# Performance work log

Hardware: AMD Instinct MI355X
Metric: run time of the kernel (lower is better)

## Reference

```python
import jax, jax.numpy as jnp
import numpy as np

B, S, H = 8, 2048, 1024

def setup_inputs() -> dict:
    key = jax.random.key(0)
    k1, k2 = jax.random.split(key)
    inputs = jax.random.normal(k1, (B, S, H), dtype=jnp.float32)
    # PyTorch Linear weight [out, in]; init ~ U(-1/sqrt(H), 1/sqrt(H)) approximated with scaled normal
    W = jax.random.normal(k2, (H, H), dtype=jnp.float32) * (1.0 / np.sqrt(H))
    b = jnp.zeros((H,), dtype=jnp.float32)
    return {"inputs": inputs, "W": W, "b": b}

def reference(inputs, W, b):
    # QW = inputs @ W^T + b   (nn.Linear)
    QW = jnp.einsum('bsh,oh->bso', inputs, W) + b  # [B,S,H]
    # score = QW @ inputs^T  (no scaling, no mask)
    score = jnp.einsum('bqh,bkh->bqk', QW, inputs)  # [B,S,S]
    attn = jax.nn.softmax(score, axis=2)
    # output = attn @ inputs
    output = jnp.einsum('bqk,bkh->bqh', attn, inputs)  # [B,S,H]
    return output
```

## Files before the change

kernel.cpp:

```cpp
#include <hip/hip_runtime.h>
#include <hip/hip_bf16.h>
#include <hip/hip_fp16.h>

typedef unsigned short u16;
typedef __attribute__((ext_vector_type(8))) _Float16 f16x8;
typedef __attribute__((ext_vector_type(4))) float f32x4;

#define B_ 8
#define S_ 2048
#define H_ 1024
#define M_ (B_ * S_)

__device__ __forceinline__ u16 f2h(float f) {
  _Float16 h = (_Float16)f;
  return __builtin_bit_cast(u16, h);
}

__global__ void f32_to_f16_kernel(const float* __restrict__ x,
                                  u16* __restrict__ o, int n4) {
  int stride = gridDim.x * blockDim.x;
  for (int i = blockIdx.x * blockDim.x + threadIdx.x; i < n4; i += stride) {
    float4 v = reinterpret_cast<const float4*>(x)[i];
    ushort4 h;
    h.x = f2h(v.x); h.y = f2h(v.y); h.z = f2h(v.z); h.w = f2h(v.w);
    reinterpret_cast<ushort4*>(o)[i] = h;
  }
}

__global__ void transpose_f32_kernel(const float* __restrict__ x,
                                     u16* __restrict__ xt) {
  __shared__ u16 t[64][65];
  int b = blockIdx.z, s0 = blockIdx.x * 64, h0 = blockIdx.y * 64;
  int tx = threadIdx.x, ty = threadIdx.y;
  const float* src = x + ((size_t)b * S_ + s0) * H_ + h0;
#pragma unroll
  for (int i = 0; i < 4; ++i)
    t[ty + 16 * i][tx] = f2h(src[(size_t)(ty + 16 * i) * H_ + tx]);
  __syncthreads();
  u16* dst = xt + ((size_t)b * H_ + h0) * S_ + s0;
#pragma unroll
  for (int i = 0; i < 4; ++i)
    dst[(size_t)(ty + 16 * i) * S_ + tx] = t[tx][ty + 16 * i];
}

__device__ __forceinline__ void async_stage16(const u16* g, u16* l) {
  __builtin_amdgcn_global_load_lds(
      (__attribute__((address_space(1))) void*)g,
      (__attribute__((address_space(3))) void*)l, 16, 0, 0);
}

template <int OM>
__global__ __launch_bounds__(512) void gemm8_kernel(
    const u16* __restrict__ A, const u16* __restrict__ B,
    float* __restrict__ Cf, u16* __restrict__ Ch,
    const float* __restrict__ bias,
    int lda, int ldb, int ldc, int K,
    long sAz, long sBz, long sCz) {
  __shared__ __align__(16) u16 sA[2][256 * 64];
  __shared__ __align__(16) u16 sB[2][256 * 64];

  int gx = gridDim.x, gy = gridDim.y;
  int nwg = gx * gy * gridDim.z;
  int wgid = blockIdx.x + gx * (blockIdx.y + gy * blockIdx.z);
  int q = nwg >> 3, r = nwg & 7;
  int xcd = wgid & 7, idx = wgid >> 3;
  int nid = (xcd < r ? xcd * (q + 1) : r * (q + 1) + (xcd - r) * q) + idx;
  int bxi = nid % gx, t2 = nid / gx;
  int byi = t2 % gy, bzi = t2 / gy;

  int tid = threadIdx.x, wave = tid >> 6, lane = tid & 63;
  int wm = wave >> 2, wn = wave & 3;
  int bm = bxi * 256, bn = byi * 256;
  long zA = (long)bzi * sAz;
  long zB = (long)bzi * sBz;
  long zC = (long)bzi * sCz;
  const u16* gA = A + zA + (size_t)bm * lda;
  const u16* gB = B + zB + (size_t)bn * ldb;

  int srow = tid >> 3;
  int scolb = (tid & 7) << 4;
  int sco = (scolb ^ ((srow & 7) << 4)) >> 1;
  size_t aO0 = (size_t)srow * lda + sco, aO1 = aO0 + (size_t)64 * lda;
  size_t bO0 = (size_t)srow * ldb + sco, bO1 = bO0 + (size_t)64 * ldb;
  int ld0 = srow * 64 + (scolb >> 1), ld1 = ld0 + 64 * 64;

  auto stgA = [&](int slot, int half, int kofs) {
    const u16* g = gA + (size_t)(half * 128) * lda + kofs;
    u16* l = &sA[slot][half * 8192];
    async_stage16(g + aO0, l + ld0);
    async_stage16(g + aO1, l + ld1);
  };
  auto stgB = [&](int slot, int half, int kofs) {
    const u16* g = gB + (size_t)(half * 128) * ldb + kofs;
    u16* l = &sB[slot][half * 8192];
    async_stage16(g + bO0, l + ld0);
    async_stage16(g + bO1, l + ld1);
  };

  int la = lane & 15;
  int kg = (lane >> 4) << 4;
  auto frag = [&](const u16* base, int row, int colb) -> f16x8 {
    int off = (row << 7) + (colb ^ ((row & 7) << 4));
    return *reinterpret_cast<const f16x8*>(
        reinterpret_cast<const char*>(base) + off);
  };

  f16x8 aF[4][2], bF[2][2];
  f32x4 acc[8][4] = {};

  auto RA = [&](int slot, int qm) {
#pragma unroll
    for (int j = 0; j < 4; ++j)
#pragma unroll
      for (int ks = 0; ks < 2; ++ks)
        aF[j][ks] = frag(sA[slot], qm * 128 + (j * 2 + wm) * 16 + la,
                         ks * 64 + kg);
  };
  auto RB = [&](int slot, int qn) {
#pragma unroll
    for (int i = 0; i < 2; ++i)
#pragma unroll
      for (int ks = 0; ks < 2; ++ks)
        bF[i][ks] = frag(sB[slot], qn * 128 + (i * 4 + wn) * 16 + la,
                         ks * 64 + kg);
  };
  auto MM = [&](int qm, int qn) {
#pragma unroll
    for (int ks = 0; ks < 2; ++ks)
#pragma unroll
      for (int j = 0; j < 4; ++j)
#pragma unroll
        for (int i = 0; i < 2; ++i)
          acc[qm * 4 + j][qn * 2 + i] = __builtin_amdgcn_mfma_f32_16x16x32_f16(
              aF[j][ks], bF[i][ks], acc[qm * 4 + j][qn * 2 + i], 0, 0, 0);
  };

#define VM4 asm volatile("s_waitcnt vmcnt(4)" ::: "memory")
#define VM2 asm volatile("s_waitcnt vmcnt(2)" ::: "memory")
#define BAR __builtin_amdgcn_s_barrier()
#define LG0                                              \
  asm volatile("s_waitcnt lgkmcnt(0)" ::: "memory");     \
  __builtin_amdgcn_sched_barrier(0)
#define MFMA_CL(qm, qn)                 \
  __builtin_amdgcn_s_setprio(1);        \
  MM(qm, qn);                           \
  __builtin_amdgcn_s_setprio(0)

  stgA(0, 0, 0); stgB(0, 0, 0); stgA(0, 1, 0); stgB(0, 1, 0);
  VM4;
  BAR;

  int NI = K >> 7;
  for (int it = 0; it < NI; ++it) {
    int k1 = (2 * it + 1) << 6, k2 = (2 * it + 2) << 6;
    bool more = (it + 1 < NI);
    RA(0, 0); RB(0, 0); stgA(1, 0, k1);
    BAR; LG0; MFMA_CL(0, 0); VM2; BAR;
    RA(0, 1); stgB(1, 0, k1);
    BAR; LG0; MFMA_CL(1, 0); BAR;
    RB(0, 1); stgA(1, 1, k1);
    BAR; LG0; MFMA_CL(1, 1); BAR;
    RA(0, 0); stgB(1, 1, k1);
    BAR; LG0; MFMA_CL(0, 1); VM4; BAR;
    RA(1, 0); RB(1, 0); if (more) stgA(0, 0, k2);
    BAR; LG0; MFMA_CL(0, 0); VM2; BAR;
    RA(1, 1); if (more) stgB(0, 0, k2);
    BAR; LG0; MFMA_CL(1, 0); BAR;
    RB(1, 1); if (more) stgA(0, 1, k2);
    BAR; LG0; MFMA_CL(1, 1); BAR;
    RA(1, 0); if (more) stgB(0, 1, k2);
    BAR; LG0; MFMA_CL(0, 1); VM4; BAR;
  }
#undef VM4
#undef VM2
#undef BAR
#undef LG0
#undef MFMA_CL

#pragma unroll
  for (int mf = 0; mf < 8; ++mf) {
    int qm = mf >> 2, j = mf & 3;
    int row = bm + qm * 128 + (j * 2 + wm) * 16 + (lane >> 4) * 4;
#pragma unroll
    for (int nf = 0; nf < 4; ++nf) {
      int qn = nf >> 1, i = nf & 1;
      int col = bn + qn * 128 + (i * 4 + wn) * 16 + la;
#pragma unroll
      for (int r = 0; r < 4; ++r) {
        float v = acc[mf][nf][r];
        if constexpr (OM == 1) {
          Ch[zC + (size_t)(row + r) * ldc + col] = f2h(v + bias[col]);
        } else {
          Cf[zC + (size_t)(row + r) * ldc + col] = v;
        }
      }
    }
  }
}

__global__ __launch_bounds__(256) void softmax_kernel(const float* __restrict__ sc,
                                                      u16* __restrict__ attn,
                                                      int opitch) {
  __shared__ float red[4];
  size_t row = blockIdx.x;
  const float* p = sc + row * S_;
  u16* o = attn + row * (size_t)opitch;
  int t = threadIdx.x;
  float4 v0 = reinterpret_cast<const float4*>(p)[t];
  float4 v1 = reinterpret_cast<const float4*>(p)[t + 256];
  float mx = fmaxf(fmaxf(fmaxf(v0.x, v0.y), fmaxf(v0.z, v0.w)),
                   fmaxf(fmaxf(v1.x, v1.y), fmaxf(v1.z, v1.w)));
#pragma unroll
  for (int d = 32; d > 0; d >>= 1) mx = fmaxf(mx, __shfl_xor(mx, d));
  if ((t & 63) == 0) red[t >> 6] = mx;
  __syncthreads();
  mx = fmaxf(fmaxf(red[0], red[1]), fmaxf(red[2], red[3]));
  float e[8];
  e[0] = __expf(v0.x - mx); e[1] = __expf(v0.y - mx);
  e[2] = __expf(v0.z - mx); e[3] = __expf(v0.w - mx);
  e[4] = __expf(v1.x - mx); e[5] = __expf(v1.y - mx);
  e[6] = __expf(v1.z - mx); e[7] = __expf(v1.w - mx);
  float s = ((e[0] + e[1]) + (e[2] + e[3])) + ((e[4] + e[5]) + (e[6] + e[7]));
#pragma unroll
  for (int d = 32; d > 0; d >>= 1) s += __shfl_xor(s, d);
  __syncthreads();
  if ((t & 63) == 0) red[t >> 6] = s;
  __syncthreads();
  s = (red[0] + red[1]) + (red[2] + red[3]);
  float inv = 1.0f / s;
  ushort4 h0, h1;
  h0.x = f2h(e[0] * inv); h0.y = f2h(e[1] * inv);
  h0.z = f2h(e[2] * inv); h0.w = f2h(e[3] * inv);
  h1.x = f2h(e[4] * inv); h1.y = f2h(e[5] * inv);
  h1.z = f2h(e[6] * inv); h1.w = f2h(e[7] * inv);
  reinterpret_cast<ushort4*>(o)[t] = h0;
  reinterpret_cast<ushort4*>(o)[t + 256] = h1;
}

extern "C" void kernel_launch(void* const* d_in, const int* in_sizes, int n_in,
                              void* d_out, int out_size, void* d_ws, size_t ws_size,
                              hipStream_t stream) {
  const float* X = (const float*)d_in[0];
  const float* W = (const float*)d_in[1];
  const float* bias = (const float*)d_in[2];
  float* out = (float*)d_out;
  char* ws = (char*)d_ws;

  const size_t MB = 1ull << 20;
  u16* XF = (u16*)(ws);
  u16* WF = (u16*)(ws + 32 * MB);
  u16* XT = (u16*)(ws + 34 * MB);
  u16* QW = (u16*)(ws + 66 * MB);
  float* SC = (float*)(ws + 98 * MB);
  u16* PF = (u16*)(ws + 162 * MB);

  int plan = (ws_size >= 226 * MB) ? 2 : (ws_size >= 163 * MB) ? 1 : 0;
  int CB = (plan >= 1) ? 4 : 2;
  int nch = B_ / CB;

  f32_to_f16_kernel<<<2048, 256, 0, stream>>>(X, XF, M_ * H_ / 4);
  f32_to_f16_kernel<<<1024, 256, 0, stream>>>(W, WF, H_ * H_ / 4);
  transpose_f32_kernel<<<dim3(S_ / 64, H_ / 64, B_), dim3(64, 16), 0, stream>>>(X, XT);
  gemm8_kernel<1><<<dim3(M_ / 256, H_ / 256, 1), 512, 0, stream>>>(
      XF, WF, nullptr, QW, bias, H_, H_, H_, H_, 0, 0, 0);
  for (int ch = 0; ch < nch; ++ch) {
    long off = (long)ch * CB;
    gemm8_kernel<0><<<dim3(S_ / 256, S_ / 256, CB), 512, 0, stream>>>(
        QW + off * S_ * H_, XF + off * S_ * H_, SC, nullptr, nullptr,
        H_, H_, S_, H_, (long)S_ * H_, (long)S_ * H_, (long)S_ * S_);
    if (plan == 2) {
      softmax_kernel<<<CB * S_, 256, 0, stream>>>(
          SC, PF + off * S_ * S_, S_);
    } else {
      softmax_kernel<<<CB * S_, 256, 0, stream>>>(
          SC, (u16*)SC, 2 * S_);
      gemm8_kernel<0><<<dim3(S_ / 256, H_ / 256, CB), 512, 0, stream>>>(
          (u16*)SC, XT + off * (long)H_ * S_,
          out + off * (long)S_ * H_, nullptr, nullptr,
          2 * S_, S_, H_, S_, (long)S_ * 2 * S_, (long)H_ * S_, (long)S_ * H_);
    }
  }
  if (plan == 2) {
    gemm8_kernel<0><<<dim3(S_ / 256, H_ / 256, B_), 512, 0, stream>>>(
        PF, XT, out, nullptr, nullptr,
        S_, S_, H_, S_, (long)S_ * S_, (long)H_ * S_, (long)S_ * H_);
  }
}
```

Before: 282.2 us.

## Fuse f16 conversion into transpose and re-pipeline GEMM main loop per K-tile

The transpose kernel now also writes the row-major f16 copy of X, so the separate f32-to-f16 pass over X, and its second full read of the input, is dropped. The GEMM main loop is restructured from a two-K-tile unrolled body into a per-64-wide K-tile loop with double-buffered slots. It reorders the fragment reads and stage loads and adjusts the vmcnt/lgkmcnt waits, aiming for better overlap of global-to-LDS copies with MFMA work. The new wait counts and slot reuse order are delicate and risk races or extra stalls. The transpose kernel's extra writes are narrow 2-byte stores, which may coalesce less well than the old vectorised conversion.

```diff
diff --git a/kernel.cpp b/kernel.cpp
--- a/kernel.cpp
+++ b/kernel.cpp
@@ -28,14 +28,19 @@
 }
 
 __global__ void transpose_f32_kernel(const float* __restrict__ x,
-                                     u16* __restrict__ xt) {
+                                     u16* __restrict__ xt,
+                                     u16* __restrict__ xf) {
   __shared__ u16 t[64][65];
   int b = blockIdx.z, s0 = blockIdx.x * 64, h0 = blockIdx.y * 64;
   int tx = threadIdx.x, ty = threadIdx.y;
   const float* src = x + ((size_t)b * S_ + s0) * H_ + h0;
-#pragma unroll
-  for (int i = 0; i < 4; ++i)
-    t[ty + 16 * i][tx] = f2h(src[(size_t)(ty + 16 * i) * H_ + tx]);
+  u16* dstf = xf + ((size_t)b * S_ + s0) * H_ + h0;
+#pragma unroll
+  for (int i = 0; i < 4; ++i) {
+    u16 h = f2h(src[(size_t)(ty + 16 * i) * H_ + tx]);
+    t[ty + 16 * i][tx] = h;
+    dstf[(size_t)(ty + 16 * i) * H_ + tx] = h;
+  }
   __syncthreads();
   u16* dst = xt + ((size_t)b * H_ + h0) * S_ + s0;
 #pragma unroll
@@ -137,6 +142,8 @@
 
 #define VM4 asm volatile("s_waitcnt vmcnt(4)" ::: "memory")
 #define VM2 asm volatile("s_waitcnt vmcnt(2)" ::: "memory")
+#define VM0 asm volatile("s_waitcnt vmcnt(0)" ::: "memory")
+#define LG8 asm volatile("s_waitcnt lgkmcnt(8)" ::: "memory")
 #define BAR __builtin_amdgcn_s_barrier()
 #define LG0                                              \
   asm volatile("s_waitcnt lgkmcnt(0)" ::: "memory");     \
@@ -146,33 +153,40 @@
   MM(qm, qn);                           \
   __builtin_amdgcn_s_setprio(0)
 
-  stgA(0, 0, 0); stgB(0, 0, 0); stgA(0, 1, 0); stgB(0, 1, 0);
+  stgA(0, 0, 0); stgB(0, 0, 0); stgB(0, 1, 0); stgA(0, 1, 0);
   VM4;
   BAR;
 
-  int NI = K >> 7;
-  for (int it = 0; it < NI; ++it) {
-    int k1 = (2 * it + 1) << 6, k2 = (2 * it + 2) << 6;
-    bool more = (it + 1 < NI);
-    RA(0, 0); RB(0, 0); stgA(1, 0, k1);
-    BAR; LG0; MFMA_CL(0, 0); VM2; BAR;
-    RA(0, 1); stgB(1, 0, k1);
-    BAR; LG0; MFMA_CL(1, 0); BAR;
-    RB(0, 1); stgA(1, 1, k1);
-    BAR; LG0; MFMA_CL(1, 1); BAR;
-    RA(0, 0); stgB(1, 1, k1);
-    BAR; LG0; MFMA_CL(0, 1); VM4; BAR;
-    RA(1, 0); RB(1, 0); if (more) stgA(0, 0, k2);
-    BAR; LG0; MFMA_CL(0, 0); VM2; BAR;
-    RA(1, 1); if (more) stgB(0, 0, k2);
-    BAR; LG0; MFMA_CL(1, 0); BAR;
-    RB(1, 1); if (more) stgA(0, 1, k2);
-    BAR; LG0; MFMA_CL(1, 1); BAR;
-    RA(1, 0); if (more) stgB(0, 1, k2);
-    BAR; LG0; MFMA_CL(0, 1); VM4; BAR;
+  int NT = K >> 6;
+  for (int t = 0; t < NT; ++t) {
+    int s = t & 1, ns = s ^ 1;
+    int kn = (t + 1) << 6;
+    bool more = (t + 1 < NT);
+    RA(s, 0); RB(s, 0);
+    if (more) stgA(ns, 0, kn);
+    LG8;
+    BAR; LG0; MFMA_CL(0, 0);
+    if (more) { VM4; } else { VM2; }
+    BAR;
+    RB(s, 1);
+    if (more) stgB(ns, 0, kn);
+    BAR; LG0; MFMA_CL(0, 1);
+    if (more) { VM4; } else { VM0; }
+    BAR;
+    RA(s, 1);
+    if (more) stgB(ns, 1, kn);
+    BAR; LG0; MFMA_CL(1, 1);
+    BAR;
+    RB(s, 0);
+    if (more) stgA(ns, 1, kn);
+    BAR; LG0; MFMA_CL(1, 0);
+    if (more) { VM4; }
+    BAR;
   }
 #undef VM4
 #undef VM2
+#undef VM0
+#undef LG8
 #undef BAR
 #undef LG0
 #undef MFMA_CL
@@ -258,9 +272,9 @@
   int CB = (plan >= 1) ? 4 : 2;
   int nch = B_ / CB;
 
-  f32_to_f16_kernel<<<2048, 256, 0, stream>>>(X, XF, M_ * H_ / 4);
   f32_to_f16_kernel<<<1024, 256, 0, stream>>>(W, WF, H_ * H_ / 4);
-  transpose_f32_kernel<<<dim3(S_ / 64, H_ / 64, B_), dim3(64, 16), 0, stream>>>(X, XT);
+  transpose_f32_kernel<<<dim3(S_ / 64, H_ / 64, B_), dim3(64, 16), 0, stream>>>(
+      X, XT, XF);
   gemm8_kernel<1><<<dim3(M_ / 256, H_ / 256, 1), 512, 0, stream>>>(
       XF, WF, nullptr, QW, bias, H_, H_, H_, H_, 0, 0, 0);
   for (int ch = 0; ch < nch; ++ch) {
```

New measurement: 265.6 us. 1.06x faster.
